# Kernel tuning notes

Measured on AMD Instinct MI355X. Metric: run time of the kernel, lower is better.

Reference implementation:

```python
import jax, jax.numpy as jnp
import numpy as np
from jax import lax

HIDDEN = 512

def _rnn_layer(xs, W_ih, W_hh, b):
    # xs: [B,T,F] -> ys: [B,T,H]; h_t = tanh(x_t W_ih^T + b + h_{t-1} W_hh^T)
    B = xs.shape[0]
    xp = jnp.einsum('btf,hf->bth', xs, W_ih) + b  # precompute input projections
    def step(h, xp_t):
        h = jnp.tanh(xp_t + h @ W_hh.T)
        return h, h
    h0 = jnp.zeros((B, W_hh.shape[0]), dtype=xs.dtype)
    _, ys = lax.scan(step, h0, xp.transpose(1, 0, 2))  # scan over time
    return ys.transpose(1, 0, 2)


def setup_inputs() -> dict:
    key = jax.random.key(0)
    ks = jax.random.split(key, 16)
    B, T, F, H, M, C = 128, 1024, 24, HIDDEN, 1024, 8
    s = 0.05  # small init to keep tanh unsaturated
    inp = {
        'x': jax.random.normal(ks[0], (B, T, F), jnp.float32),
        'W_ih0': jax.random.normal(ks[1], (H, F), jnp.float32) * s,
        'W_hh0': jax.random.normal(ks[2], (H, H), jnp.float32) * s,
        'b_ih0': jnp.zeros((H,), jnp.float32),
        'b_hh0': jnp.zeros((H,), jnp.float32),
        'W_ih1': jax.random.normal(ks[3], (H, H), jnp.float32) * s,
        'W_hh1': jax.random.normal(ks[4], (H, H), jnp.float32) * s,
        'b_ih1': jnp.zeros((H,), jnp.float32),
        'b_hh1': jnp.zeros((H,), jnp.float32),
        'W_ih2': jax.random.normal(ks[5], (H, H), jnp.float32) * s,
        'W_hh2': jax.random.normal(ks[6], (H, H), jnp.float32) * s,
        'b_ih2': jnp.zeros((H,), jnp.float32),
        'b_hh2': jnp.zeros((H,), jnp.float32),
        'W1': jax.random.normal(ks[7], (M, H), jnp.float32) * s,
        'b1': jnp.zeros((M,), jnp.float32),
        'W2': jax.random.normal(ks[8], (C, M), jnp.float32) * s,
        'b2': jnp.zeros((C,), jnp.float32),
    }
    return inp


def reference(x, W_ih0, W_hh0, b_ih0, b_hh0, W_ih1, W_hh1, b_ih1, b_hh1,
              W_ih2, W_hh2, b_ih2, b_hh2, W1, b1, W2, b2):
    h = _rnn_layer(x, W_ih0, W_hh0, b_ih0 + b_hh0)
    h = _rnn_layer(h, W_ih1, W_hh1, b_ih1 + b_hh1)
    h = _rnn_layer(h, W_ih2, W_hh2, b_ih2 + b_hh2)
    last = h[:, -1, :]  # [B,H] last timestep of top layer
    z = last @ W1.T + b1
    z = jax.nn.silu(z)
    return z @ W2.T + b2
```

## Files before the change

### kernel.cpp

```cpp
#include <hip/hip_runtime.h>
#include <cstdint>
#include <cstddef>


typedef _Float16 half_t;
typedef __attribute__((ext_vector_type(2))) _Float16 half2_t;
typedef __attribute__((ext_vector_type(8))) _Float16 frag8;
typedef __attribute__((ext_vector_type(4))) float    frag4;

union U32H2 { unsigned u; half2_t h2; };

__device__ __forceinline__ float fast_tanh(float x) {
    float ax = __builtin_fabsf(x);
    float e  = __expf(-2.f * ax);
    float r  = (1.f - e) / (1.f + e);
    return __builtin_copysignf(r, x);
}

#define WN (512 * 512)

__global__ __launch_bounds__(256) void k_cvt(
    const float* whh0, const float* whh1, const float* whh2,
    const float* wih1, const float* wih2,
    const float* bi0, const float* bh0, const float* bi1, const float* bh1,
    const float* bi2, const float* bh2,
    half_t* w16, float* bias)
{
    int idx = blockIdx.x * 256 + threadIdx.x;
    if (idx < 5 * WN) {
        int seg = idx / WN, off = idx % WN;
        const float* s = seg == 0 ? whh0 : seg == 1 ? whh1 : seg == 2 ? whh2
                       : seg == 3 ? wih1 : wih2;
        w16[idx] = (half_t)s[off];
    } else {
        int j = idx - 5 * WN;
        if (j < 3 * 512) {
            int l = j >> 9, o = j & 511;
            const float* a = l == 0 ? bi0 : l == 1 ? bi1 : bi2;
            const float* c = l == 0 ? bh0 : l == 1 ? bh1 : bh2;
            bias[j] = a[o] + c[o];
        }
    }
}

__global__ __launch_bounds__(256) void k_xp0(
    const float* __restrict__ x, const float* __restrict__ wih0,
    const float* __restrict__ bias0, half_t* __restrict__ P)
{
    __shared__ float wl[512 * 25];
    __shared__ float xl[32 * 25];
    int tid = threadIdx.x;
    int r0  = blockIdx.x * 32;
    for (int i = tid; i < 512 * 24; i += 256) {
        int o = i / 24, f = i - o * 24;
        wl[o * 25 + f] = wih0[i];
    }
    for (int i = tid; i < 32 * 24; i += 256) {
        int r = i / 24, f = i - r * 24;
        xl[r * 25 + f] = x[(size_t)(r0 + r) * 24 + f];
    }
    __syncthreads();
    int r = tid >> 3, c = tid & 7;
    float xr[24];
#pragma unroll
    for (int f = 0; f < 24; f++) xr[f] = xl[r * 25 + f];
    size_t orow = (size_t)(r0 + r) * 512;
    for (int og = 0; og < 8; og++) {
        half_t hv[8];
#pragma unroll
        for (int oj = 0; oj < 8; oj++) {
            int o = og * 64 + c * 8 + oj;
            float acc = bias0[o];
#pragma unroll
            for (int f = 0; f < 24; f++) acc = fmaf(xr[f], wl[o * 25 + f], acc);
            hv[oj] = (half_t)acc;
        }
        *(uint4*)(P + orow + og * 64 + c * 8) = *(const uint4*)hv;
    }
}

__global__ __launch_bounds__(512, 2) void k_scan(
    half_t* __restrict__ P, const half_t* __restrict__ whh)
{
    extern __shared__ char smem[];
    frag8*    wlds = (frag8*)smem;
    unsigned* hbuf = (unsigned*)(smem + 65536);

    int tid  = threadIdx.x;
    int w    = tid >> 6, lane = tid & 63;
    int col  = lane & 15, quad = lane >> 4;
    int b    = blockIdx.x;

    frag8 areg[4][14];
#pragma unroll
    for (int mt = 0; mt < 4; mt++) {
        int out = w * 64 + mt * 16 + col;
        const half_t* wr = whh + (size_t)out * 512 + quad * 8;
#pragma unroll
        for (int kb = 0; kb < 14; kb++)
            areg[mt][kb] = *(const frag8*)(wr + kb * 32);
#pragma unroll
        for (int i = 0; i < 2; i++)
            wlds[(w * 8 + i * 4 + mt) * 64 + lane] = *(const frag8*)(wr + (14 + i) * 32);
    }
    if (tid < 256) { hbuf[tid] = 0u; hbuf[256 + tid] = 0u; }
    __syncthreads();

    half_t* Pb = P + (size_t)b * 1024 * 512;
    int  out0 = w * 64 + col * 16 + quad * 4;
    bool act  = (col < 4);
    uint2 xq = make_uint2(0u, 0u);
    if (act) xq = *(const uint2*)(Pb + out0);
    int cur = 0;
    for (int t = 0; t < 1024; t++) {
        const uint4* hb4 = (const uint4*)(hbuf + cur * 256);
        frag4 acc[4];
#pragma unroll
        for (int mt = 0; mt < 4; mt++) acc[mt] = (frag4){0.f, 0.f, 0.f, 0.f};
#pragma unroll
        for (int kb = 0; kb < 14; kb++) {
            uint4 bu = hb4[kb * 4 + quad];
            frag8 bf = *(const frag8*)&bu;
#pragma unroll
            for (int mt = 0; mt < 4; mt++)
                acc[mt] = __builtin_amdgcn_mfma_f32_16x16x32_f16(
                    areg[mt][kb], bf, acc[mt], 0, 0, 0);
        }
#pragma unroll
        for (int i = 0; i < 2; i++) {
            uint4 bu = hb4[(14 + i) * 4 + quad];
            frag8 bf = *(const frag8*)&bu;
#pragma unroll
            for (int mt = 0; mt < 4; mt++) {
                frag8 a = wlds[(w * 8 + i * 4 + mt) * 64 + lane];
                acc[mt] = __builtin_amdgcn_mfma_f32_16x16x32_f16(
                    a, bf, acc[mt], 0, 0, 0);
            }
        }
        if (act) {
            int tn = (t + 1 < 1024) ? t + 1 : 1023;
            uint2 xn = *(const uint2*)(Pb + (size_t)tn * 512 + out0);
            float y0 = 0.f, y1 = 0.f, y2 = 0.f, y3 = 0.f;
#pragma unroll
            for (int mt = 0; mt < 4; mt++)
                if (col == mt) { y0 = acc[mt][0]; y1 = acc[mt][1];
                                 y2 = acc[mt][2]; y3 = acc[mt][3]; }
            U32H2 lo, hi; lo.u = xq.x; hi.u = xq.y;
            U32H2 ho, h1;
            ho.h2.x = (half_t)fast_tanh(y0 + (float)lo.h2.x);
            ho.h2.y = (half_t)fast_tanh(y1 + (float)lo.h2.y);
            h1.h2.x = (half_t)fast_tanh(y2 + (float)hi.h2.x);
            h1.h2.y = (half_t)fast_tanh(y3 + (float)hi.h2.y);
            uint2 hv = make_uint2(ho.u, h1.u);
            *(uint2*)&hbuf[(cur ^ 1) * 256 + (out0 >> 1)] = hv;
            *(uint2*)(Pb + (size_t)t * 512 + out0) = hv;
            xq = xn;
        }
        __syncthreads();
        cur ^= 1;
    }
}

__global__ __launch_bounds__(256, 2) void k_proj(
    half_t* __restrict__ P, const half_t* __restrict__ w16,
    const float* __restrict__ bias)
{
    extern __shared__ char smem[];
    half_t* A = (half_t*)smem;
    const int AS = 520;
    int tid = threadIdx.x;
    size_t r0 = (size_t)blockIdx.x * 64;

    const uint4* Pg = (const uint4*)(P + r0 * 512);
    for (int u = tid; u < 4096; u += 256) {
        uint4 v = Pg[u];
        int row = u >> 6, c = u & 63;
        *(uint4*)(A + row * AS + c * 8) = v;
    }
    __syncthreads();

    int wave = tid >> 6, lane = tid & 63;
    int lm = lane & 15, lq = lane >> 4;

    frag4 acc[4][8];
#pragma unroll
    for (int mt = 0; mt < 4; mt++)
#pragma unroll
        for (int nt = 0; nt < 8; nt++) acc[mt][nt] = (frag4){0.f, 0.f, 0.f, 0.f};

    for (int kb = 0; kb < 16; kb++) {
        int k0 = kb * 32 + lq * 8;
        frag8 af[4];
#pragma unroll
        for (int mt = 0; mt < 4; mt++)
            af[mt] = *(const frag8*)(A + (mt * 16 + lm) * AS + k0);
        frag8 bf[8];
#pragma unroll
        for (int nt = 0; nt < 8; nt++) {
            int n = wave * 128 + nt * 16 + lm;
            bf[nt] = *(const frag8*)(w16 + (size_t)n * 512 + k0);
        }
#pragma unroll
        for (int mt = 0; mt < 4; mt++)
#pragma unroll
            for (int nt = 0; nt < 8; nt++)
                acc[mt][nt] = __builtin_amdgcn_mfma_f32_16x16x32_f16(
                    af[mt], bf[nt], acc[mt][nt], 0, 0, 0);
    }

#pragma unroll
    for (int mt = 0; mt < 4; mt++) {
        int row = mt * 16 + lq * 4;
#pragma unroll
        for (int nt = 0; nt < 8; nt++) {
            int oc = wave * 128 + nt * 16 + lm;
            float bo = bias[oc];
#pragma unroll
            for (int i = 0; i < 4; i++) {
                float v = acc[mt][nt][i] + bo;
                P[(r0 + row + i) * 512 + oc] = (half_t)v;
            }
        }
    }
}

__global__ __launch_bounds__(256) void k_head(
    const half_t* __restrict__ P, const float* __restrict__ W1,
    const float* __restrict__ b1, const float* __restrict__ W2,
    const float* __restrict__ b2, float* __restrict__ out)
{
    __shared__ float lastv[512];
    __shared__ float zl[1024];
    __shared__ float red[8][33];
    int tid = threadIdx.x, b = blockIdx.x;
    const half_t* lr = P + ((size_t)b * 1024 + 1023) * 512;
    lastv[tid]       = (float)lr[tid];
    lastv[tid + 256] = (float)lr[tid + 256];
    __syncthreads();
#pragma unroll
    for (int i = 0; i < 4; i++) {
        int m = tid + 256 * i;
        const float* wr = W1 + (size_t)m * 512;
        float acc = b1[m];
        for (int k = 0; k < 512; k += 4) {
            float4 wv = *(const float4*)(wr + k);
            acc = fmaf(wv.x, lastv[k],     acc);
            acc = fmaf(wv.y, lastv[k + 1], acc);
            acc = fmaf(wv.z, lastv[k + 2], acc);
            acc = fmaf(wv.w, lastv[k + 3], acc);
        }
        zl[m] = acc / (1.f + __expf(-acc));
    }
    __syncthreads();
    int c = tid & 7, mc = tid >> 3;
    float p = 0.f;
#pragma unroll
    for (int j = 0; j < 32; j++) {
        int m = mc * 32 + j;
        p = fmaf(zl[m], W2[c * 1024 + m], p);
    }
    red[c][mc] = p;
    __syncthreads();
    if (tid < 8) {
        float s = b2[tid];
#pragma unroll
        for (int j = 0; j < 32; j++) s += red[tid][j];
        out[b * 8 + tid] = s;
    }
}

extern "C" void kernel_launch(void* const* d_in, const int* in_sizes, int n_in,
                              void* d_out, int out_size, void* d_ws, size_t ws_size,
                              hipStream_t stream)
{
    const float* x    = (const float*)d_in[0];
    const float* wih0 = (const float*)d_in[1];
    const float* whh0 = (const float*)d_in[2];
    const float* bi0  = (const float*)d_in[3];
    const float* bh0  = (const float*)d_in[4];
    const float* wih1 = (const float*)d_in[5];
    const float* whh1 = (const float*)d_in[6];
    const float* bi1  = (const float*)d_in[7];
    const float* bh1  = (const float*)d_in[8];
    const float* wih2 = (const float*)d_in[9];
    const float* whh2 = (const float*)d_in[10];
    const float* bi2  = (const float*)d_in[11];
    const float* bh2  = (const float*)d_in[12];
    const float* W1   = (const float*)d_in[13];
    const float* b1   = (const float*)d_in[14];
    const float* W2   = (const float*)d_in[15];
    const float* b2   = (const float*)d_in[16];
    float* out = (float*)d_out;

    char* ws = (char*)d_ws;
    half_t* P    = (half_t*)ws;
    half_t* W16  = (half_t*)(ws + 134217728);
    float*  bias = (float*)(ws + 134217728 + 2621440);

    hipFuncSetAttribute((const void*)k_scan,
                        hipFuncAttributeMaxDynamicSharedMemorySize, 67584);
    hipFuncSetAttribute((const void*)k_proj,
                        hipFuncAttributeMaxDynamicSharedMemorySize, 66560);

    k_cvt<<<5126, 256, 0, stream>>>(whh0, whh1, whh2, wih1, wih2,
                                    bi0, bh0, bi1, bh1, bi2, bh2, W16, bias);
    k_xp0<<<4096, 256, 0, stream>>>(x, wih0, bias, P);
    k_scan<<<128, 512, 67584, stream>>>(P, W16 + 0 * WN);
    k_proj<<<2048, 256, 66560, stream>>>(P, W16 + 3 * WN, bias + 512);
    k_scan<<<128, 512, 67584, stream>>>(P, W16 + 1 * WN);
    k_proj<<<2048, 256, 66560, stream>>>(P, W16 + 4 * WN, bias + 1024);
    k_scan<<<128, 512, 67584, stream>>>(P, W16 + 2 * WN);
    k_head<<<128, 256, 0, stream>>>(P, W1, b1, W2, b2, out);
}
```

Before: 6.369 ms.

## Split scan across 16 waves with full W_hh held in registers

Result: slower. 10.96 ms (+72.0%).

```diff
diff --git a/kernel.cpp b/kernel.cpp
--- a/kernel.cpp
+++ b/kernel.cpp
@@ -79,80 +79,59 @@
     }
 }
 
-__global__ __launch_bounds__(512, 2) void k_scan(
+__global__ __launch_bounds__(1024) void k_scan(
     half_t* __restrict__ P, const half_t* __restrict__ whh)
 {
-    extern __shared__ char smem[];
-    frag8*    wlds = (frag8*)smem;
-    unsigned* hbuf = (unsigned*)(smem + 65536);
+    __shared__ unsigned hbuf[2][256];
 
     int tid  = threadIdx.x;
     int w    = tid >> 6, lane = tid & 63;
     int col  = lane & 15, quad = lane >> 4;
     int b    = blockIdx.x;
 
-    frag8 areg[4][14];
-#pragma unroll
-    for (int mt = 0; mt < 4; mt++) {
-        int out = w * 64 + mt * 16 + col;
+    frag8 areg[2][16];
+#pragma unroll
+    for (int i = 0; i < 2; i++) {
+        int out = w * 32 + i * 16 + col;
         const half_t* wr = whh + (size_t)out * 512 + quad * 8;
 #pragma unroll
-        for (int kb = 0; kb < 14; kb++)
-            areg[mt][kb] = *(const frag8*)(wr + kb * 32);
-#pragma unroll
-        for (int i = 0; i < 2; i++)
-            wlds[(w * 8 + i * 4 + mt) * 64 + lane] = *(const frag8*)(wr + (14 + i) * 32);
-    }
-    if (tid < 256) { hbuf[tid] = 0u; hbuf[256 + tid] = 0u; }
+        for (int kb = 0; kb < 16; kb++)
+            areg[i][kb] = *(const frag8*)(wr + kb * 32);
+    }
+    if (tid < 256) { hbuf[0][tid] = 0u; hbuf[1][tid] = 0u; }
     __syncthreads();
 
     half_t* Pb = P + (size_t)b * 1024 * 512;
-    int  out0 = w * 64 + col * 16 + quad * 4;
-    bool act  = (col < 4);
+    bool act  = (col < 2);
+    int  out0 = w * 32 + col * 16 + quad * 4;
     uint2 xq = make_uint2(0u, 0u);
     if (act) xq = *(const uint2*)(Pb + out0);
     int cur = 0;
     for (int t = 0; t < 1024; t++) {
-        const uint4* hb4 = (const uint4*)(hbuf + cur * 256);
-        frag4 acc[4];
-#pragma unroll
-        for (int mt = 0; mt < 4; mt++) acc[mt] = (frag4){0.f, 0.f, 0.f, 0.f};
-#pragma unroll
-        for (int kb = 0; kb < 14; kb++) {
+        const uint4* hb4 = (const uint4*)hbuf[cur];
+        frag4 acc0 = (frag4){0.f, 0.f, 0.f, 0.f};
+        frag4 acc1 = (frag4){0.f, 0.f, 0.f, 0.f};
+#pragma unroll
+        for (int kb = 0; kb < 16; kb++) {
             uint4 bu = hb4[kb * 4 + quad];
             frag8 bf = *(const frag8*)&bu;
-#pragma unroll
-            for (int mt = 0; mt < 4; mt++)
-                acc[mt] = __builtin_amdgcn_mfma_f32_16x16x32_f16(
-                    areg[mt][kb], bf, acc[mt], 0, 0, 0);
-        }
-#pragma unroll
-        for (int i = 0; i < 2; i++) {
-            uint4 bu = hb4[(14 + i) * 4 + quad];
-            frag8 bf = *(const frag8*)&bu;
-#pragma unroll
-            for (int mt = 0; mt < 4; mt++) {
-                frag8 a = wlds[(w * 8 + i * 4 + mt) * 64 + lane];
-                acc[mt] = __builtin_amdgcn_mfma_f32_16x16x32_f16(
-                    a, bf, acc[mt], 0, 0, 0);
-            }
+            acc0 = __builtin_amdgcn_mfma_f32_16x16x32_f16(
+                areg[0][kb], bf, acc0, 0, 0, 0);
+            acc1 = __builtin_amdgcn_mfma_f32_16x16x32_f16(
+                areg[1][kb], bf, acc1, 0, 0, 0);
         }
         if (act) {
             int tn = (t + 1 < 1024) ? t + 1 : 1023;
             uint2 xn = *(const uint2*)(Pb + (size_t)tn * 512 + out0);
-            float y0 = 0.f, y1 = 0.f, y2 = 0.f, y3 = 0.f;
-#pragma unroll
-            for (int mt = 0; mt < 4; mt++)
-                if (col == mt) { y0 = acc[mt][0]; y1 = acc[mt][1];
-                                 y2 = acc[mt][2]; y3 = acc[mt][3]; }
+            frag4 y = (col == 0) ? acc0 : acc1;
             U32H2 lo, hi; lo.u = xq.x; hi.u = xq.y;
-            U32H2 ho, h1;
-            ho.h2.x = (half_t)fast_tanh(y0 + (float)lo.h2.x);
-            ho.h2.y = (half_t)fast_tanh(y1 + (float)lo.h2.y);
-            h1.h2.x = (half_t)fast_tanh(y2 + (float)hi.h2.x);
-            h1.h2.y = (half_t)fast_tanh(y3 + (float)hi.h2.y);
-            uint2 hv = make_uint2(ho.u, h1.u);
-            *(uint2*)&hbuf[(cur ^ 1) * 256 + (out0 >> 1)] = hv;
+            U32H2 h0, h1;
+            h0.h2.x = (half_t)fast_tanh(y[0] + (float)lo.h2.x);
+            h0.h2.y = (half_t)fast_tanh(y[1] + (float)lo.h2.y);
+            h1.h2.x = (half_t)fast_tanh(y[2] + (float)hi.h2.x);
+            h1.h2.y = (half_t)fast_tanh(y[3] + (float)hi.h2.y);
+            uint2 hv = make_uint2(h0.u, h1.u);
+            *(uint2*)&hbuf[cur ^ 1][out0 >> 1] = hv;
             *(uint2*)(Pb + (size_t)t * 512 + out0) = hv;
             xq = xn;
         }
@@ -297,18 +276,16 @@
     half_t* W16  = (half_t*)(ws + 134217728);
     float*  bias = (float*)(ws + 134217728 + 2621440);
 
-    hipFuncSetAttribute((const void*)k_scan,
-                        hipFuncAttributeMaxDynamicSharedMemorySize, 67584);
     hipFuncSetAttribute((const void*)k_proj,
                         hipFuncAttributeMaxDynamicSharedMemorySize, 66560);
 
     k_cvt<<<5126, 256, 0, stream>>>(whh0, whh1, whh2, wih1, wih2,
                                     bi0, bh0, bi1, bh1, bi2, bh2, W16, bias);
     k_xp0<<<4096, 256, 0, stream>>>(x, wih0, bias, P);
-    k_scan<<<128, 512, 67584, stream>>>(P, W16 + 0 * WN);
+    k_scan<<<128, 1024, 0, stream>>>(P, W16 + 0 * WN);
     k_proj<<<2048, 256, 66560, stream>>>(P, W16 + 3 * WN, bias + 512);
-    k_scan<<<128, 512, 67584, stream>>>(P, W16 + 1 * WN);
+    k_scan<<<128, 1024, 0, stream>>>(P, W16 + 1 * WN);
     k_proj<<<2048, 256, 66560, stream>>>(P, W16 + 4 * WN, bias + 1024);
-    k_scan<<<128, 512, 67584, stream>>>(P, W16 + 2 * WN);
+    k_scan<<<128, 1024, 0, stream>>>(P, W16 + 2 * WN);
     k_head<<<128, 256, 0, stream>>>(P, W1, b1, W2, b2, out);
 }
```
